# Kernel tuning notes

Hardware: AMD Instinct MI355X
Metric: run time of the kernel (lower is better)

Reference implementation:

```python
import jax, jax.numpy as jnp
import numpy as np

B, T, N, D = 4, 128, 512, 32
CHEB_K, EMB, HEADS, TA_LAYERS, GCN_NUM, TCN_BLOCKS, KSIZE = 3, 10, 2, 2, 3, 3, 3


def setup_inputs() -> dict:
    key = jax.random.key(0)
    ks = jax.random.split(key, 12)
    x = jax.random.normal(ks[0], (B, T, N, D), jnp.float32)
    init_state = jnp.zeros((1, B, N, D), jnp.float32)  # unused by forward, kept for signature fidelity
    node_embeddings = jax.random.normal(ks[1], (N, EMB), jnp.float32)
    a = jax.random.uniform(ks[2], (N, N), jnp.float32)
    a = 0.5 * (a + a.T)
    adj = a / jnp.sum(a, axis=1, keepdims=True)  # row-normalized dense adjacency
    s = 0.05
    gcn_w = jax.random.normal(ks[3], (GCN_NUM, EMB, CHEB_K, D, D), jnp.float32) * s
    gcn_b = jax.random.normal(ks[4], (GCN_NUM, EMB, D), jnp.float32) * s
    tcn_w1 = jax.random.normal(ks[5], (TCN_BLOCKS, D, D, KSIZE), jnp.float32) * s
    tcn_b1 = jnp.zeros((TCN_BLOCKS, D), jnp.float32)
    tcn_w2 = jax.random.normal(ks[6], (TCN_BLOCKS, D, D, KSIZE), jnp.float32) * s
    tcn_b2 = jnp.zeros((TCN_BLOCKS, D), jnp.float32)
    ta_wq = jax.random.normal(ks[7], (TA_LAYERS, D, D), jnp.float32) * s
    ta_wk = jax.random.normal(ks[8], (TA_LAYERS, D, D), jnp.float32) * s
    ta_wv = jax.random.normal(ks[9], (TA_LAYERS, D, D), jnp.float32) * s
    ta_wo = jax.random.normal(ks[10], (TA_LAYERS, D, D), jnp.float32) * s
    ta_g = jnp.ones((TA_LAYERS, D), jnp.float32)
    ta_b = jnp.zeros((TA_LAYERS, D), jnp.float32)
    return dict(x=x, init_state=init_state, node_embeddings=node_embeddings, adj=adj,
                gcn_w=gcn_w, gcn_b=gcn_b, tcn_w1=tcn_w1, tcn_b1=tcn_b1, tcn_w2=tcn_w2,
                tcn_b2=tcn_b2, ta_wq=ta_wq, ta_wk=ta_wk, ta_wv=ta_wv, ta_wo=ta_wo,
                ta_g=ta_g, ta_b=ta_b)


def _cheb_supports(adj, k):
    I = jnp.eye(adj.shape[0], dtype=adj.dtype)
    s = [I, adj]
    for _ in range(2, k):
        s.append(2.0 * (adj @ s[-1]) - s[-2])
    return jnp.stack(s[:k])  # (k, N, N)


def _emb_gcn(h, supports, E, wp, bp):
    # h: (B,T,N,C); supports: (k,N,N); E: (N,EMB); wp: (EMB,k,C,O); bp: (EMB,O)
    xg = jnp.einsum('knm,btmc->btknc', supports, h)
    W = jnp.einsum('ne,ekco->nkco', E, wp)       # per-node Chebyshev weights
    bias = E @ bp                                 # (N,O)
    return jnp.einsum('btknc,nkco->btno', xg, W) + bias


def _causal_conv(y, w, b, dil):
    # y: (BN, C, T); w: (O, C, K)
    pad = (w.shape[-1] - 1) * dil
    out = jax.lax.conv_general_dilated(y, w, (1,), [(pad, 0)], rhs_dilation=(dil,),
                                       dimension_numbers=('NCH', 'OIH', 'NCH'))
    return out + b[None, :, None]


def _temporal_block(y, w1, b1, w2, b2, dil):
    o = jax.nn.relu(_causal_conv(y, w1, b1, dil))
    o = jax.nn.relu(_causal_conv(o, w2, b2, dil))
    return jax.nn.relu(o + y)  # residual (in_ch == out_ch)


def _layernorm(h, g, b):
    mu = jnp.mean(h, -1, keepdims=True)
    var = jnp.var(h, -1, keepdims=True)
    return (h - mu) * jax.lax.rsqrt(var + 1e-5) * g + b


def _attn_layer(h, wq, wk, wv, wo, g, b):
    # h: (BN, T, D) temporal self-attention
    bn, t, d = h.shape
    dh = d // HEADS
    scale = 1.0 / float(np.sqrt(dh))
    q = (h @ wq).reshape(bn, t, HEADS, dh)
    k = (h @ wk).reshape(bn, t, HEADS, dh)
    v = (h @ wv).reshape(bn, t, HEADS, dh)
    a = jax.nn.softmax(jnp.einsum('bqhd,bkhd->bhqk', q, k) * scale, axis=-1)
    o = jnp.einsum('bhqk,bkhd->bqhd', a, v).reshape(bn, t, d) @ wo
    return _layernorm(h + o, g, b)


def reference(x, init_state, node_embeddings, adj, gcn_w, gcn_b, tcn_w1, tcn_b1,
              tcn_w2, tcn_b2, ta_wq, ta_wk, ta_wv, ta_wo, ta_g, ta_b):
    supports = _cheb_supports(adj, CHEB_K)
    h = x
    for i in range(GCN_NUM):  # 3 stacked EmbGCN layers, vectorized over time
        h = _emb_gcn(h, supports, node_embeddings, gcn_w[i], gcn_b[i])
    b, t, n, d = h.shape
    y = jnp.transpose(h, (0, 2, 3, 1)).reshape(b * n, d, t)  # (BN, D, T)
    for i in range(TCN_BLOCKS):  # dilations 1,2,4
        y = _temporal_block(y, tcn_w1[i], tcn_b1[i], tcn_w2[i], tcn_b2[i], 2 ** i)
    h2 = jnp.transpose(y.reshape(b, n, d, t), (0, 1, 3, 2)).reshape(b * n, t, d)
    for i in range(TA_LAYERS):
        h2 = _attn_layer(h2, ta_wq[i], ta_wk[i], ta_wv[i], ta_wo[i], ta_g[i], ta_b[i])
    return jnp.transpose(h2.reshape(b, n, t, d), (0, 2, 1, 3))  # (B,T,N,D)
```

## Files before the change

kernel.cpp:

```cpp
#include <hip/hip_runtime.h>
#include <hip/hip_bf16.h>


typedef __attribute__((ext_vector_type(8))) short short8;
typedef __attribute__((ext_vector_type(4))) short short4v;
typedef __attribute__((ext_vector_type(4))) float float4v;

#define MFMA32(a, b, c) __builtin_amdgcn_mfma_f32_16x16x32_bf16((a), (b), (c), 0, 0, 0)
#if defined(__has_builtin)
#if __has_builtin(__builtin_amdgcn_mfma_f32_16x16x16_bf16)
#define MFMA16A(a, b, c) __builtin_amdgcn_mfma_f32_16x16x16_bf16((a), (b), (c), 0, 0, 0)
#endif
#endif
#ifndef MFMA16A
#define MFMA16A(a, b, c) __builtin_amdgcn_mfma_f32_16x16x16bf16_1k((a), (b), (c), 0, 0, 0)
#endif

#if defined(__has_builtin)
#if __has_builtin(__builtin_amdgcn_exp2f)
#define EXP2F(x) __builtin_amdgcn_exp2f(x)
#endif
#endif
#ifndef EXP2F
#define EXP2F(x) exp2f(x)
#endif

typedef const __attribute__((address_space(1))) unsigned int* gas_ptr;
typedef __attribute__((address_space(3))) unsigned int* las_ptr;
__device__ __forceinline__ void glds16(const void* g, void* l) {
  __builtin_amdgcn_global_load_lds((gas_ptr)g, (las_ptr)l, 16, 0, 0);
}

__device__ __forceinline__ unsigned short f2b(float f) {
  unsigned int x = __float_as_uint(f);
  unsigned int r = (x + 0x7fffu + ((x >> 16) & 1u)) >> 16;
  return (unsigned short)r;
}
__device__ __forceinline__ float b2f(unsigned short u) {
  return __uint_as_float(((unsigned int)u) << 16);
}
__device__ __forceinline__ unsigned int f2b2(float lo, float hi) {
  union { __hip_bfloat162 h; unsigned int u; } cv;
  cv.h = __float22bfloat162_rn(make_float2(lo, hi));
  return cv.u;
}
__device__ __forceinline__ ushort4 f2b4(float a, float b, float c, float d) {
  union { unsigned int u[2]; ushort4 s; } cv;
  cv.u[0] = f2b2(a, b);
  cv.u[1] = f2b2(c, d);
  return cv.s;
}

__global__ void __launch_bounds__(256) prep_supports(
    const float* __restrict__ adj, unsigned short* __restrict__ Sb) {
  __shared__ float arow[512];
  int n = blockIdx.x, tid = threadIdx.x;
  for (int m = tid; m < 512; m += 256) {
    float v = adj[n * 512 + m];
    arow[m] = v;
    Sb[n * 512 + m] = f2b(v);
  }
  __syncthreads();
  for (int m = tid; m < 512; m += 256) {
    float acc = 0.f;
    for (int p = 0; p < 512; ++p) acc += arow[p] * adj[p * 512 + m];
    Sb[(512 + n) * 512 + m] = f2b(2.f * acc - (m == n ? 1.f : 0.f));
  }
}

__global__ void __launch_bounds__(256) prep_w_kernel(
    const float* __restrict__ emb, const float* __restrict__ gw,
    const float* __restrict__ gb,
    unsigned short* __restrict__ W8, float* __restrict__ biasn) {
  int bid = blockIdx.x;
  int i = bid >> 9, n = bid & 511, tid = threadIdx.x;
  float ev[10];
#pragma unroll
  for (int e = 0; e < 10; ++e) ev[e] = emb[n * 10 + e];
  for (int idx = tid; idx < 3072; idx += 256) {
    int s = idx >> 10, c = (idx >> 5) & 31, o = idx & 31;
    float acc = 0.f;
#pragma unroll
    for (int e = 0; e < 10; ++e) acc += ev[e] * gw[(i * 10 + e) * 3072 + idx];
    W8[((i * 512 + n) * 3 + s) * 1024 + (c >> 3) * 256 + o * 8 + (c & 7)] =
        f2b(acc);
  }
  if (tid < 32) {
    float acc = 0.f;
#pragma unroll
    for (int e = 0; e < 10; ++e) acc += ev[e] * gb[(i * 10 + e) * 32 + tid];
    biasn[(i * 512 + n) * 32 + tid] = acc;
  }
}

__global__ void __launch_bounds__(256) prep_tw(
    const float* __restrict__ w1g, const float* __restrict__ w2g,
    unsigned short* __restrict__ Wt) {
  int bid = blockIdx.x;
  int blk = bid >> 1, conv = bid & 1;
  const float* w = (conv ? w2g : w1g) + blk * 3072;
  for (int idx = threadIdx.x; idx < 3072; idx += 256) {
    int kk = idx >> 10, rem = idx & 1023;
    int o = rem >> 5, c = rem & 31;
    Wt[bid * 3072 + idx] = f2b(w[o * 96 + c * 3 + kk]);
  }
}

__global__ void __launch_bounds__(256) prep_attn_w(
    const float* __restrict__ wqg, const float* __restrict__ wkg,
    const float* __restrict__ wvg, const float* __restrict__ wog,
    unsigned short* __restrict__ Wf) {
  int idx = blockIdx.x * 256 + threadIdx.x;
  if (idx >= 8192) return;
  int L = idx >> 12;
  int mat = (idx >> 10) & 3;
  int nt = (idx >> 9) & 1;
  int lane = (idx >> 3) & 63;
  int j = idx & 7;
  int quad = lane >> 4, l15 = lane & 15;
  const float* base =
      (mat == 0 ? wqg : mat == 1 ? wkg : mat == 2 ? wvg : wog) + L * 1024;
  float v = base[(quad * 8 + j) * 32 + nt * 16 + l15];
  if (mat == 0) v *= 0.36067376022224085f;
  Wf[idx] = f2b(v);
}

__global__ void __launch_bounds__(256) conv_x(
    const float* __restrict__ x, unsigned short* __restrict__ H8,
    unsigned short* __restrict__ Hrm) {
  int bid = blockIdx.x;
  int nblk = bid >> 3, part = bid & 7;
  int tid = threadIdx.x;
  for (int qq = tid; qq < 2048; qq += 256) {
    int q = part * 2048 + qq;
    int bt = q >> 5, c = q & 31;
    const float* xb = x + bt * 16384 + nblk * 256 + c;
    float f[8];
#pragma unroll
    for (int s = 0; s < 8; ++s) f[s] = xb[s * 32];
    union { unsigned int u[4]; uint4 v; } pk;
    pk.u[0] = f2b2(f[0], f[1]);
    pk.u[1] = f2b2(f[2], f[3]);
    pk.u[2] = f2b2(f[4], f[5]);
    pk.u[3] = f2b2(f[6], f[7]);
    *(uint4*)&H8[nblk * 131072 + q * 8] = pk.v;
  }
  for (int qq = tid; qq < 2048; qq += 256) {
    int q = part * 2048 + qq;
    int s = q >> 11, e0 = (q & 2047) * 8;
    int bt = e0 >> 5, c0 = e0 & 31;
    const float* xb = x + bt * 16384 + (nblk * 8 + s) * 32 + c0;
    float4 v0 = *(const float4*)&xb[0];
    float4 v1 = *(const float4*)&xb[4];
    union { unsigned int u[4]; uint4 v; } pk;
    pk.u[0] = f2b2(v0.x, v0.y);
    pk.u[1] = f2b2(v0.z, v0.w);
    pk.u[2] = f2b2(v1.x, v1.y);
    pk.u[3] = f2b2(v1.z, v1.w);
    *(uint4*)&Hrm[(nblk * 8 + s) * 16384 + e0] = pk.v;
  }
}

__global__ void __launch_bounds__(256) gcn_phaseA(
    const unsigned short* __restrict__ Sb,
    const unsigned short* __restrict__ H8,
    unsigned short* __restrict__ G) {
  __shared__ unsigned short As[2][128 * 32];
  __shared__ unsigned short Bs[2][4096];
  int bid0 = blockIdx.x;
  int nb = (bid0 & 7) * 128 + (bid0 >> 3);
  int mt = nb & 7, jt = nb >> 3;
  int m0 = mt * 128, j0 = jt * 128;
  int tid = threadIdx.x;
  int wave = tid >> 6, lane = tid & 63;
  int wm = wave >> 1, wj = wave & 1;
  int l15 = lane & 15, quad = lane >> 4;
  float4v acc[4][4];
#pragma unroll
  for (int a = 0; a < 4; ++a)
#pragma unroll
    for (int b = 0; b < 4; ++b) acc[a][b] = (float4v)0.f;
#pragma unroll
  for (int p = 0; p < 2; ++p) {
    int q = tid + p * 256;
    int m = q >> 2;
    int c8 = (q & 3) ^ ((q >> 3) & 3);
    glds16(&Sb[(m0 + m) * 512 + c8 * 8], &As[0][q * 8]);
  }
  {
    const unsigned short* hb = H8 + j0 * 8;
#pragma unroll
    for (int p = 0; p < 2; ++p) {
      int q = tid + p * 256;
      glds16(&hb[(q >> 7) * 131072 + (q & 127) * 8], &Bs[0][q * 8]);
    }
  }
  __syncthreads();
#pragma unroll 2
  for (int it = 0; it < 16; ++it) {
    int cur = it & 1;
    if (it < 15) {
      int ncn = (it + 1) * 32;
#pragma unroll
      for (int p = 0; p < 2; ++p) {
        int q = tid + p * 256;
        int m = q >> 2;
        int c8 = (q & 3) ^ ((q >> 3) & 3);
        glds16(&Sb[(m0 + m) * 512 + ncn + c8 * 8], &As[cur ^ 1][q * 8]);
      }
      const unsigned short* hb = H8 + (ncn >> 3) * 131072 + j0 * 8;
#pragma unroll
      for (int p = 0; p < 2; ++p) {
        int q = tid + p * 256;
        glds16(&hb[(q >> 7) * 131072 + (q & 127) * 8], &Bs[cur ^ 1][q * 8]);
      }
    }
    short8 af[4], bfr[4];
#pragma unroll
    for (int mi = 0; mi < 4; ++mi) {
      int row = wm * 64 + mi * 16 + l15;
      int c8 = quad ^ ((row >> 1) & 3);
      af[mi] = *(const short8*)&As[cur][row * 32 + c8 * 8];
    }
#pragma unroll
    for (int ji = 0; ji < 4; ++ji)
      bfr[ji] =
          *(const short8*)&Bs[cur][quad * 1024 + (wj * 64 + ji * 16 + l15) * 8];
#pragma unroll
    for (int mi = 0; mi < 4; ++mi)
#pragma unroll
      for (int ji = 0; ji < 4; ++ji)
        acc[mi][ji] = MFMA32(af[mi], bfr[ji], acc[mi][ji]);
    __syncthreads();
  }
#pragma unroll
  for (int mi = 0; mi < 4; ++mi)
#pragma unroll
    for (int ji = 0; ji < 4; ++ji) {
      int j = j0 + wj * 64 + ji * 16 + l15;
#pragma unroll
      for (int r = 0; r < 4; ++r) {
        int m = m0 + wm * 64 + mi * 16 + quad * 4 + r;
        G[m * 16384 + j] = f2b(acc[mi][ji][r]);
      }
    }
}

__global__ void __launch_bounds__(256) gcn_phaseB(
    const unsigned short* __restrict__ Hrm, const unsigned short* __restrict__ G,
    const unsigned short* __restrict__ W8, const float* __restrict__ biasn,
    unsigned short* __restrict__ H8out, unsigned short* __restrict__ Hrmout,
    unsigned short* __restrict__ tcnout) {
  int bid = blockIdx.x;
  int n = bid >> 1, bh = bid & 1;
  int tid = threadIdx.x;
  int lane = tid & 63, wave = tid >> 6, l15 = lane & 15, quad = lane >> 4;
  short8 wb[3][2];
#pragma unroll
  for (int s = 0; s < 3; ++s)
#pragma unroll
    for (int nt = 0; nt < 2; ++nt)
      wb[s][nt] = *(const short8*)&W8[(n * 3 + s) * 1024 + quad * 256 +
                                      (nt * 16 + l15) * 8];
  float b0 = biasn[n * 32 + l15], b1 = biasn[n * 32 + 16 + l15];
  int n8base = (n >> 3) * 131072 + (n & 7);
#pragma unroll
  for (int mi = 0; mi < 4; ++mi) {
    int bt0 = bh * 256 + wave * 64 + mi * 16;
    int btl = bt0 + l15;
    short8 a0 = *(const short8*)&Hrm[n * 16384 + btl * 32 + quad * 8];
    short8 a1 = *(const short8*)&G[n * 16384 + btl * 32 + quad * 8];
    short8 a2 = *(const short8*)&G[(512 + n) * 16384 + btl * 32 + quad * 8];
    float4v acc0 = MFMA32(a0, wb[0][0], (float4v)0.f);
    acc0 = MFMA32(a1, wb[1][0], acc0);
    acc0 = MFMA32(a2, wb[2][0], acc0);
    float4v acc1 = MFMA32(a0, wb[0][1], (float4v)0.f);
    acc1 = MFMA32(a1, wb[1][1], acc1);
    acc1 = MFMA32(a2, wb[2][1], acc1);
#pragma unroll
    for (int r = 0; r < 4; ++r) {
      int bt = bt0 + quad * 4 + r;
      unsigned short v0 = f2b(acc0[r] + b0);
      unsigned short v1 = f2b(acc1[r] + b1);
      if (tcnout) {
        int bb = bt >> 7, t = bt & 127;
        int o0 = l15, o1 = 16 + l15;
        tcnout[n * 16384 + bb * 4096 + (o0 >> 3) * 1024 + t * 8 + (o0 & 7)] = v0;
        tcnout[n * 16384 + bb * 4096 + (o1 >> 3) * 1024 + t * 8 + (o1 & 7)] = v1;
      } else {
        H8out[n8base + (bt * 32 + l15) * 8] = v0;
        H8out[n8base + (bt * 32 + 16 + l15) * 8] = v1;
        Hrmout[n * 16384 + bt * 32 + l15] = v0;
        Hrmout[n * 16384 + bt * 32 + 16 + l15] = v1;
      }
    }
  }
}

__global__ void __launch_bounds__(256) tcn_kernel(
    const unsigned short* __restrict__ Yin, unsigned short* __restrict__ yout,
    const unsigned short* __restrict__ Wt,
    const float* __restrict__ b1g, const float* __restrict__ b2g) {
  __shared__ unsigned short Y8[4][4352];
  __shared__ unsigned short O8[4][4352];
  int tid = threadIdx.x, wave = tid >> 6, lane = tid & 63;
  int l15 = lane & 15, quad = lane >> 4;
  int n = blockIdx.x, b = wave;
  unsigned short* y8 = &Y8[wave][0];
  unsigned short* o8 = &O8[wave][0];
  {
    int cg = lane >> 4, t = (lane >> 1) & 7, half = lane & 1;
    ushort4 z = {0, 0, 0, 0};
    *(ushort4*)&y8[(cg * 136 + t) * 8 + half * 4] = z;
    *(ushort4*)&o8[(cg * 136 + t) * 8 + half * 4] = z;
  }
  const unsigned short* src = Yin + n * 16384 + b * 4096;
#pragma unroll
  for (int p = 0; p < 8; ++p) {
    int e = p * 64 + lane;
    int cg = e >> 7, t = e & 127;
    *(uint4*)&y8[(cg * 136 + t + 8) * 8] = *(const uint4*)&src[e * 8];
  }
  for (int blk = 0; blk < 3; ++blk) {
    int dil = 1 << blk;
    for (int conv = 0; conv < 2; ++conv) {
      const unsigned short* wbase = Wt + ((blk * 2 + conv) * 3) * 1024;
      short8 af[2][3];
#pragma unroll
      for (int mt = 0; mt < 2; ++mt)
#pragma unroll
        for (int kk = 0; kk < 3; ++kk)
          af[mt][kk] = *(const short8*)&wbase[kk * 1024 +
                                              (mt * 16 + l15) * 32 + quad * 8];
      const float* bias = (conv ? b2g : b1g) + blk * 32;
      float4 bs0 = *(const float4*)&bias[quad * 4];
      float4 bs1 = *(const float4*)&bias[16 + quad * 4];
      float bb0[4] = {bs0.x, bs0.y, bs0.z, bs0.w};
      float bb1[4] = {bs1.x, bs1.y, bs1.z, bs1.w};
      const unsigned short* rbuf = conv ? o8 : y8;
#pragma unroll 2
      for (int nt = 0; nt < 8; ++nt) {
        float4v acc0 = (float4v)0.f, acc1 = (float4v)0.f;
#pragma unroll
        for (int kk = 0; kk < 3; ++kk) {
          int tb = nt * 16 + l15 + 8 - (2 - kk) * dil;
          short8 bf = *(const short8*)&rbuf[(quad * 136 + tb) * 8];
          acc0 = MFMA32(af[0][kk], bf, acc0);
          acc1 = MFMA32(af[1][kk], bf, acc1);
        }
        int t8 = nt * 16 + l15 + 8;
        int og0 = (quad >> 1), ci0 = (quad & 1) * 4;
        if (conv == 0) {
          ushort4 w0 = f2b4(fmaxf(acc0[0] + bb0[0], 0.f),
                            fmaxf(acc0[1] + bb0[1], 0.f),
                            fmaxf(acc0[2] + bb0[2], 0.f),
                            fmaxf(acc0[3] + bb0[3], 0.f));
          ushort4 w1 = f2b4(fmaxf(acc1[0] + bb1[0], 0.f),
                            fmaxf(acc1[1] + bb1[1], 0.f),
                            fmaxf(acc1[2] + bb1[2], 0.f),
                            fmaxf(acc1[3] + bb1[3], 0.f));
          *(ushort4*)&o8[((og0)*136 + t8) * 8 + ci0] = w0;
          *(ushort4*)&o8[((2 + og0) * 136 + t8) * 8 + ci0] = w1;
        } else {
          ushort4 y0 = *(const ushort4*)&y8[((og0)*136 + t8) * 8 + ci0];
          ushort4 y1 = *(const ushort4*)&y8[((2 + og0) * 136 + t8) * 8 + ci0];
          ushort4 w0 = f2b4(
              fmaxf(fmaxf(acc0[0] + bb0[0], 0.f) + b2f(y0.x), 0.f),
              fmaxf(fmaxf(acc0[1] + bb0[1], 0.f) + b2f(y0.y), 0.f),
              fmaxf(fmaxf(acc0[2] + bb0[2], 0.f) + b2f(y0.z), 0.f),
              fmaxf(fmaxf(acc0[3] + bb0[3], 0.f) + b2f(y0.w), 0.f));
          ushort4 w1 = f2b4(
              fmaxf(fmaxf(acc1[0] + bb1[0], 0.f) + b2f(y1.x), 0.f),
              fmaxf(fmaxf(acc1[1] + bb1[1], 0.f) + b2f(y1.y), 0.f),
              fmaxf(fmaxf(acc1[2] + bb1[2], 0.f) + b2f(y1.z), 0.f),
              fmaxf(fmaxf(acc1[3] + bb1[3], 0.f) + b2f(y1.w), 0.f));
          *(ushort4*)&y8[((og0)*136 + t8) * 8 + ci0] = w0;
          *(ushort4*)&y8[((2 + og0) * 136 + t8) * 8 + ci0] = w1;
        }
      }
    }
  }
  unsigned short* dst = yout + n * 16384 + b * 4096;
#pragma unroll
  for (int p = 0; p < 8; ++p) {
    int e = p * 64 + lane;
    int og = e >> 7, t = e & 127;
    *(uint4*)&dst[t * 32 + og * 8] = *(const uint4*)&y8[(og * 136 + t + 8) * 8];
  }
}

__global__ void __launch_bounds__(256) attn_kernel(
    const unsigned short* __restrict__ yin,
    float* __restrict__ outp,
    const unsigned short* __restrict__ Wf,
    const float* __restrict__ gg, const float* __restrict__ bgb) {
  __shared__ unsigned short hfrag[4096];
  __shared__ unsigned short KbOb[5120];
  __shared__ unsigned short QT[32 * 136];
  __shared__ unsigned short VT[32 * 136];
  int bn = blockIdx.x, tid = threadIdx.x;
  int b = bn >> 9, n = bn & 511;
  int lane = tid & 63, wave = tid >> 6;
  int l15 = lane & 15, quad = lane >> 4;
  int mt0 = wave * 2;

  const unsigned short* src = yin + n * 16384 + b * 4096;
  for (int q = tid; q < 512; q += 256) {
    int t = ((q >> 6) << 4) | (q & 15);
    int cb = (q >> 4) & 3;
    glds16(&src[(t * 4 + cb) * 8], &hfrag[q * 8]);
  }

  for (int L = 0; L < 2; ++L) {
    short8 wf[4][2];
#pragma unroll
    for (int mat = 0; mat < 4; ++mat)
#pragma unroll
      for (int nt = 0; nt < 2; ++nt)
        wf[mat][nt] =
            *(const short8*)&Wf[(((L * 4 + mat) * 2 + nt) * 64 + lane) * 8];
    __syncthreads();
#pragma unroll
    for (int mm = 0; mm < 2; ++mm) {
      int mtq = mt0 + mm;
      short8 af = *(const short8*)&hfrag[(mtq * 4 + quad) * 128 + l15 * 8];
      int tbase = mtq * 16 + quad * 4;
#pragma unroll
      for (int nt = 0; nt < 2; ++nt) {
        float4v qa = MFMA32(af, wf[0][nt], (float4v)0.f);
        float4v ka = MFMA32(af, wf[1][nt], (float4v)0.f);
        float4v va = MFMA32(af, wf[2][nt], (float4v)0.f);
        int d = nt * 16 + l15;
#pragma unroll
        for (int r = 0; r < 4; ++r) KbOb[(tbase + r) * 36 + d] = f2b(ka[r]);
        *(ushort4*)&QT[d * 136 + tbase] = f2b4(qa[0], qa[1], qa[2], qa[3]);
        *(ushort4*)&VT[d * 136 + tbase] = f2b4(va[0], va[1], va[2], va[3]);
      }
    }
    __syncthreads();
    float4v oaccT[2][2];
#pragma unroll
    for (int mm = 0; mm < 2; ++mm)
#pragma unroll
      for (int hh = 0; hh < 2; ++hh) oaccT[mm][hh] = (float4v)0.f;
    for (int hh = 0; hh < 2; ++hh) {
#pragma unroll
      for (int mm = 0; mm < 2; ++mm) {
        int mtq = mt0 + mm;
        short4v qb;
#pragma unroll
        for (int jj = 0; jj < 4; ++jj)
          qb[jj] = (short)QT[(hh * 16 + quad * 4 + jj) * 136 + mtq * 16 + l15];
        float4v sacc[8];
#pragma unroll
        for (int st = 0; st < 8; ++st) {
          short4v ka = *(const short4v*)&KbOb[(st * 16 + l15) * 36 + hh * 16 +
                                              quad * 4];
          sacc[st] = MFMA16A(ka, qb, (float4v)0.f);
        }
        float tmx[8];
#pragma unroll
        for (int st = 0; st < 8; ++st)
          tmx[st] = fmaxf(fmaxf(sacc[st][0], sacc[st][1]),
                          fmaxf(sacc[st][2], sacc[st][3]));
        float mx = fmaxf(fmaxf(fmaxf(tmx[0], tmx[1]), fmaxf(tmx[2], tmx[3])),
                         fmaxf(fmaxf(tmx[4], tmx[5]), fmaxf(tmx[6], tmx[7])));
        mx = fmaxf(mx, __shfl_xor(mx, 16));
        mx = fmaxf(mx, __shfl_xor(mx, 32));
        float ps[8];
#pragma unroll
        for (int st = 0; st < 8; ++st) {
#pragma unroll
          for (int r = 0; r < 4; ++r) sacc[st][r] = EXP2F(sacc[st][r] - mx);
          ps[st] = (sacc[st][0] + sacc[st][1]) + (sacc[st][2] + sacc[st][3]);
        }
        float sum = ((ps[0] + ps[1]) + (ps[2] + ps[3])) +
                    ((ps[4] + ps[5]) + (ps[6] + ps[7]));
        sum += __shfl_xor(sum, 16);
        sum += __shfl_xor(sum, 32);
        float inv = 1.f / sum;
#pragma unroll
        for (int st = 0; st < 8; ++st) {
          union { unsigned int u[2]; short4v s; } pv;
          pv.u[0] = f2b2(sacc[st][0], sacc[st][1]);
          pv.u[1] = f2b2(sacc[st][2], sacc[st][3]);
          short4v va = *(const short4v*)&VT[(hh * 16 + l15) * 136 + st * 16 +
                                            quad * 4];
          oaccT[mm][hh] = MFMA16A(va, pv.s, oaccT[mm][hh]);
        }
#pragma unroll
        for (int r = 0; r < 4; ++r) oaccT[mm][hh][r] *= inv;
      }
    }
    __syncthreads();
#pragma unroll
    for (int mm = 0; mm < 2; ++mm) {
      int mtq = mt0 + mm;
#pragma unroll
      for (int hh = 0; hh < 2; ++hh)
        *(ushort4*)&KbOb[(mtq * 16 + l15) * 40 + hh * 16 + quad * 4] =
            f2b4(oaccT[mm][hh][0], oaccT[mm][hh][1], oaccT[mm][hh][2],
                 oaccT[mm][hh][3]);
    }
    float gam0 = gg[L * 32 + l15], bet0 = bgb[L * 32 + l15];
    float gam1 = gg[L * 32 + 16 + l15], bet1 = bgb[L * 32 + 16 + l15];
#pragma unroll
    for (int mm = 0; mm < 2; ++mm) {
      int mtq = mt0 + mm;
      short8 ofa = *(const short8*)&KbOb[(mtq * 16 + l15) * 40 + quad * 8];
      float4v racc0 = MFMA32(ofa, wf[3][0], (float4v)0.f);
      float4v racc1 = MFMA32(ofa, wf[3][1], (float4v)0.f);
      int hi0 = (mtq * 4 + (l15 >> 3)) * 128 + (l15 & 7);
      int hi1 = (mtq * 4 + 2 + (l15 >> 3)) * 128 + (l15 & 7);
#pragma unroll
      for (int r = 0; r < 4; ++r) {
        int t = mtq * 16 + quad * 4 + r;
        int ro = (quad * 4 + r) * 8;
        float v0 = racc0[r] + b2f(hfrag[hi0 + ro]);
        float v1 = racc1[r] + b2f(hfrag[hi1 + ro]);
        float s = v0 + v1;
        for (int m = 1; m < 16; m <<= 1) s += __shfl_xor(s, m);
        float mu = s * 0.03125f;
        float d0 = v0 - mu, d1 = v1 - mu;
        float q = d0 * d0 + d1 * d1;
        for (int m = 1; m < 16; m <<= 1) q += __shfl_xor(q, m);
        float rs = rsqrtf(q * 0.03125f + 1e-5f);
        float y0 = d0 * rs * gam0 + bet0;
        float y1 = d1 * rs * gam1 + bet1;
        if (L == 0) {
          hfrag[hi0 + ro] = f2b(y0);
          hfrag[hi1 + ro] = f2b(y1);
        } else {
          outp[((b * 128 + t) * 512 + n) * 32 + l15] = y0;
          outp[((b * 128 + t) * 512 + n) * 32 + 16 + l15] = y1;
        }
      }
    }
  }
}

extern "C" void kernel_launch(void* const* d_in, const int* in_sizes, int n_in,
                              void* d_out, int out_size, void* d_ws, size_t ws_size,
                              hipStream_t stream) {
  const float* x    = (const float*)d_in[0];
  const float* emb  = (const float*)d_in[2];
  const float* adj  = (const float*)d_in[3];
  const float* gw   = (const float*)d_in[4];
  const float* gb   = (const float*)d_in[5];
  const float* tw1  = (const float*)d_in[6];
  const float* tb1  = (const float*)d_in[7];
  const float* tw2  = (const float*)d_in[8];
  const float* tb2  = (const float*)d_in[9];
  const float* wq   = (const float*)d_in[10];
  const float* wk   = (const float*)d_in[11];
  const float* wv   = (const float*)d_in[12];
  const float* wo   = (const float*)d_in[13];
  const float* tg   = (const float*)d_in[14];
  const float* tbb  = (const float*)d_in[15];
  float* outp = (float*)d_out;

  char* p = (char*)d_ws;
  unsigned short* Sb  = (unsigned short*)p; p += 1048576;
  unsigned short* W8  = (unsigned short*)p; p += 9437184;
  float* biasn        = (float*)p;          p += 196608;
  unsigned short* G   = (unsigned short*)p; p += 33554432;
  unsigned short* H8a = (unsigned short*)p; p += 16777216;
  unsigned short* H8b = (unsigned short*)p; p += 16777216;
  unsigned short* Hra = (unsigned short*)p; p += 16777216;
  unsigned short* Hrb = (unsigned short*)p; p += 16777216;
  unsigned short* Wt  = (unsigned short*)p; p += 36864;
  unsigned short* Wf  = (unsigned short*)p; p += 16384;

  prep_supports<<<dim3(512), dim3(256), 0, stream>>>(adj, Sb);
  prep_w_kernel<<<dim3(1536), dim3(256), 0, stream>>>(emb, gw, gb, W8, biasn);
  prep_tw<<<dim3(6), dim3(256), 0, stream>>>(tw1, tw2, Wt);
  prep_attn_w<<<dim3(32), dim3(256), 0, stream>>>(wq, wk, wv, wo, Wf);
  conv_x<<<dim3(512), dim3(256), 0, stream>>>(x, H8a, Hra);

  gcn_phaseA<<<dim3(1024), dim3(256), 0, stream>>>(Sb, H8a, G);
  gcn_phaseB<<<dim3(1024), dim3(256), 0, stream>>>(
      Hra, G, W8, biasn, H8b, Hrb, (unsigned short*)nullptr);
  gcn_phaseA<<<dim3(1024), dim3(256), 0, stream>>>(Sb, H8b, G);
  gcn_phaseB<<<dim3(1024), dim3(256), 0, stream>>>(
      Hrb, G, W8 + 1572864, biasn + 16384, H8a, Hra, (unsigned short*)nullptr);
  gcn_phaseA<<<dim3(1024), dim3(256), 0, stream>>>(Sb, H8a, G);
  gcn_phaseB<<<dim3(1024), dim3(256), 0, stream>>>(
      Hra, G, W8 + 3145728, biasn + 32768, (unsigned short*)nullptr,
      (unsigned short*)nullptr, H8b);

  tcn_kernel<<<dim3(512), dim3(256), 0, stream>>>(H8b, H8a, Wt, tb1, tb2);
  attn_kernel<<<dim3(2048), dim3(256), 0, stream>>>(H8a, outp, Wf, tg, tbb);
}
```

Baseline: 415.5 us.

## Merge prep kernels into one launch and compute adj squared with MFMA

Folds the five preprocessing kernels (supports, GCN weights, TCN weights, attention weights, input conversion) into a single kernel that dispatches on block index ranges, cutting four launches. The adj@adj product for the second Chebyshev support moves from a scalar fp32 loop to a tiled bf16 MFMA GEMM over 16 blocks. f2b now uses the hardware bf16 conversion path. The squared support is computed from bf16-rounded inputs, so it is less precise, and only 16 blocks do the GEMM, which may leave it on the critical path.

```diff
diff --git a/kernel.cpp b/kernel.cpp
--- a/kernel.cpp
+++ b/kernel.cpp
@@ -31,18 +31,16 @@
   __builtin_amdgcn_global_load_lds((gas_ptr)g, (las_ptr)l, 16, 0, 0);
 }
 
-__device__ __forceinline__ unsigned short f2b(float f) {
-  unsigned int x = __float_as_uint(f);
-  unsigned int r = (x + 0x7fffu + ((x >> 16) & 1u)) >> 16;
-  return (unsigned short)r;
-}
-__device__ __forceinline__ float b2f(unsigned short u) {
-  return __uint_as_float(((unsigned int)u) << 16);
-}
 __device__ __forceinline__ unsigned int f2b2(float lo, float hi) {
   union { __hip_bfloat162 h; unsigned int u; } cv;
   cv.h = __float22bfloat162_rn(make_float2(lo, hi));
   return cv.u;
+}
+__device__ __forceinline__ unsigned short f2b(float f) {
+  return (unsigned short)f2b2(f, f);
+}
+__device__ __forceinline__ float b2f(unsigned short u) {
+  return __uint_as_float(((unsigned int)u) << 16);
 }
 __device__ __forceinline__ ushort4 f2b4(float a, float b, float c, float d) {
   union { unsigned int u[2]; ushort4 s; } cv;
@@ -51,113 +49,168 @@
   return cv.s;
 }
 
-__global__ void __launch_bounds__(256) prep_supports(
-    const float* __restrict__ adj, unsigned short* __restrict__ Sb) {
-  __shared__ float arow[512];
-  int n = blockIdx.x, tid = threadIdx.x;
-  for (int m = tid; m < 512; m += 256) {
-    float v = adj[n * 512 + m];
-    arow[m] = v;
-    Sb[n * 512 + m] = f2b(v);
-  }
-  __syncthreads();
-  for (int m = tid; m < 512; m += 256) {
-    float acc = 0.f;
-    for (int p = 0; p < 512; ++p) acc += arow[p] * adj[p * 512 + m];
-    Sb[(512 + n) * 512 + m] = f2b(2.f * acc - (m == n ? 1.f : 0.f));
-  }
-}
-
-__global__ void __launch_bounds__(256) prep_w_kernel(
+__global__ void __launch_bounds__(256) prep_all(
+    const float* __restrict__ adj, unsigned short* __restrict__ Sb,
     const float* __restrict__ emb, const float* __restrict__ gw,
-    const float* __restrict__ gb,
-    unsigned short* __restrict__ W8, float* __restrict__ biasn) {
-  int bid = blockIdx.x;
-  int i = bid >> 9, n = bid & 511, tid = threadIdx.x;
-  float ev[10];
-#pragma unroll
-  for (int e = 0; e < 10; ++e) ev[e] = emb[n * 10 + e];
-  for (int idx = tid; idx < 3072; idx += 256) {
-    int s = idx >> 10, c = (idx >> 5) & 31, o = idx & 31;
-    float acc = 0.f;
-#pragma unroll
-    for (int e = 0; e < 10; ++e) acc += ev[e] * gw[(i * 10 + e) * 3072 + idx];
-    W8[((i * 512 + n) * 3 + s) * 1024 + (c >> 3) * 256 + o * 8 + (c & 7)] =
-        f2b(acc);
-  }
-  if (tid < 32) {
-    float acc = 0.f;
-#pragma unroll
-    for (int e = 0; e < 10; ++e) acc += ev[e] * gb[(i * 10 + e) * 32 + tid];
-    biasn[(i * 512 + n) * 32 + tid] = acc;
-  }
-}
-
-__global__ void __launch_bounds__(256) prep_tw(
+    const float* __restrict__ gb, unsigned short* __restrict__ W8,
+    float* __restrict__ biasn,
     const float* __restrict__ w1g, const float* __restrict__ w2g,
-    unsigned short* __restrict__ Wt) {
-  int bid = blockIdx.x;
-  int blk = bid >> 1, conv = bid & 1;
-  const float* w = (conv ? w2g : w1g) + blk * 3072;
-  for (int idx = threadIdx.x; idx < 3072; idx += 256) {
-    int kk = idx >> 10, rem = idx & 1023;
-    int o = rem >> 5, c = rem & 31;
-    Wt[bid * 3072 + idx] = f2b(w[o * 96 + c * 3 + kk]);
-  }
-}
-
-__global__ void __launch_bounds__(256) prep_attn_w(
+    unsigned short* __restrict__ Wt,
     const float* __restrict__ wqg, const float* __restrict__ wkg,
     const float* __restrict__ wvg, const float* __restrict__ wog,
-    unsigned short* __restrict__ Wf) {
-  int idx = blockIdx.x * 256 + threadIdx.x;
-  if (idx >= 8192) return;
-  int L = idx >> 12;
-  int mat = (idx >> 10) & 3;
-  int nt = (idx >> 9) & 1;
-  int lane = (idx >> 3) & 63;
-  int j = idx & 7;
-  int quad = lane >> 4, l15 = lane & 15;
-  const float* base =
-      (mat == 0 ? wqg : mat == 1 ? wkg : mat == 2 ? wvg : wog) + L * 1024;
-  float v = base[(quad * 8 + j) * 32 + nt * 16 + l15];
-  if (mat == 0) v *= 0.36067376022224085f;
-  Wf[idx] = f2b(v);
-}
-
-__global__ void __launch_bounds__(256) conv_x(
+    unsigned short* __restrict__ Wf,
     const float* __restrict__ x, unsigned short* __restrict__ H8,
     unsigned short* __restrict__ Hrm) {
-  int bid = blockIdx.x;
-  int nblk = bid >> 3, part = bid & 7;
-  int tid = threadIdx.x;
-  for (int qq = tid; qq < 2048; qq += 256) {
-    int q = part * 2048 + qq;
-    int bt = q >> 5, c = q & 31;
-    const float* xb = x + bt * 16384 + nblk * 256 + c;
-    float f[8];
-#pragma unroll
-    for (int s = 0; s < 8; ++s) f[s] = xb[s * 32];
-    union { unsigned int u[4]; uint4 v; } pk;
-    pk.u[0] = f2b2(f[0], f[1]);
-    pk.u[1] = f2b2(f[2], f[3]);
-    pk.u[2] = f2b2(f[4], f[5]);
-    pk.u[3] = f2b2(f[6], f[7]);
-    *(uint4*)&H8[nblk * 131072 + q * 8] = pk.v;
-  }
-  for (int qq = tid; qq < 2048; qq += 256) {
-    int q = part * 2048 + qq;
-    int s = q >> 11, e0 = (q & 2047) * 8;
-    int bt = e0 >> 5, c0 = e0 & 31;
-    const float* xb = x + bt * 16384 + (nblk * 8 + s) * 32 + c0;
-    float4 v0 = *(const float4*)&xb[0];
-    float4 v1 = *(const float4*)&xb[4];
-    union { unsigned int u[4]; uint4 v; } pk;
-    pk.u[0] = f2b2(v0.x, v0.y);
-    pk.u[1] = f2b2(v0.z, v0.w);
-    pk.u[2] = f2b2(v1.x, v1.y);
-    pk.u[3] = f2b2(v1.z, v1.w);
-    *(uint4*)&Hrm[(nblk * 8 + s) * 16384 + e0] = pk.v;
+  __shared__ unsigned short Asq[128 * 40];
+  __shared__ unsigned short Bsq[128 * 40];
+  int bid = blockIdx.x, tid = threadIdx.x;
+
+  if (bid < 64) {
+    int base = bid * 4096;
+#pragma unroll
+    for (int it = 0; it < 4; ++it) {
+      int e = base + it * 1024 + tid * 4;
+      float4 v = *(const float4*)&adj[e];
+      union { unsigned int u[2]; ushort4 s; } pk;
+      pk.u[0] = f2b2(v.x, v.y);
+      pk.u[1] = f2b2(v.z, v.w);
+      *(ushort4*)&Sb[e] = pk.s;
+    }
+    return;
+  }
+  if (bid < 80) {
+    int tb = bid - 64;
+    int mt = tb >> 2, jt = tb & 3;
+    int m0 = mt * 128, j0 = jt * 128;
+    int wave = tid >> 6, lane = tid & 63;
+    int wm = wave >> 1, wj = wave & 1;
+    int l15 = lane & 15, quad = lane >> 4;
+    float4v acc[4][4];
+#pragma unroll
+    for (int a = 0; a < 4; ++a)
+#pragma unroll
+      for (int b = 0; b < 4; ++b) acc[a][b] = (float4v)0.f;
+    for (int kt = 0; kt < 512; kt += 32) {
+#pragma unroll
+      for (int p = 0; p < 16; ++p) {
+        int idx = p * 256 + tid;
+        int m = idx >> 5, k = idx & 31;
+        Asq[m * 40 + k] = f2b(adj[(m0 + m) * 512 + kt + k]);
+      }
+#pragma unroll
+      for (int p = 0; p < 16; ++p) {
+        int idx = p * 256 + tid;
+        int k = idx >> 7, j = idx & 127;
+        Bsq[j * 40 + k] = f2b(adj[(kt + k) * 512 + j0 + j]);
+      }
+      __syncthreads();
+      short8 af[4], bfr[4];
+#pragma unroll
+      for (int mi = 0; mi < 4; ++mi)
+        af[mi] = *(const short8*)&Asq[(wm * 64 + mi * 16 + l15) * 40 + quad * 8];
+#pragma unroll
+      for (int ji = 0; ji < 4; ++ji)
+        bfr[ji] = *(const short8*)&Bsq[(wj * 64 + ji * 16 + l15) * 40 + quad * 8];
+#pragma unroll
+      for (int mi = 0; mi < 4; ++mi)
+#pragma unroll
+        for (int ji = 0; ji < 4; ++ji)
+          acc[mi][ji] = MFMA32(af[mi], bfr[ji], acc[mi][ji]);
+      __syncthreads();
+    }
+#pragma unroll
+    for (int mi = 0; mi < 4; ++mi)
+#pragma unroll
+      for (int ji = 0; ji < 4; ++ji) {
+        int j = j0 + wj * 64 + ji * 16 + l15;
+#pragma unroll
+        for (int r = 0; r < 4; ++r) {
+          int m = m0 + wm * 64 + mi * 16 + quad * 4 + r;
+          Sb[(512 + m) * 512 + j] =
+              f2b(2.f * acc[mi][ji][r] - (m == j ? 1.f : 0.f));
+        }
+      }
+    return;
+  }
+  if (bid < 1616) {
+    int b2 = bid - 80;
+    int i = b2 >> 9, n = b2 & 511;
+    float ev[10];
+#pragma unroll
+    for (int e = 0; e < 10; ++e) ev[e] = emb[n * 10 + e];
+    for (int idx = tid; idx < 3072; idx += 256) {
+      int s = idx >> 10, c = (idx >> 5) & 31, o = idx & 31;
+      float acc = 0.f;
+#pragma unroll
+      for (int e = 0; e < 10; ++e) acc += ev[e] * gw[(i * 10 + e) * 3072 + idx];
+      W8[((i * 512 + n) * 3 + s) * 1024 + (c >> 3) * 256 + o * 8 + (c & 7)] =
+          f2b(acc);
+    }
+    if (tid < 32) {
+      float acc = 0.f;
+#pragma unroll
+      for (int e = 0; e < 10; ++e) acc += ev[e] * gb[(i * 10 + e) * 32 + tid];
+      biasn[(i * 512 + n) * 32 + tid] = acc;
+    }
+    return;
+  }
+  if (bid < 1622) {
+    int b2 = bid - 1616;
+    int blk = b2 >> 1, conv = b2 & 1;
+    const float* w = (conv ? w2g : w1g) + blk * 3072;
+    for (int idx = tid; idx < 3072; idx += 256) {
+      int kk = idx >> 10, rem = idx & 1023;
+      int o = rem >> 5, c = rem & 31;
+      Wt[b2 * 3072 + idx] = f2b(w[o * 96 + c * 3 + kk]);
+    }
+    return;
+  }
+  if (bid < 1654) {
+    int idx = (bid - 1622) * 256 + tid;
+    int L = idx >> 12;
+    int mat = (idx >> 10) & 3;
+    int nt = (idx >> 9) & 1;
+    int lane = (idx >> 3) & 63;
+    int j = idx & 7;
+    int quad = lane >> 4, l15 = lane & 15;
+    const float* base =
+        (mat == 0 ? wqg : mat == 1 ? wkg : mat == 2 ? wvg : wog) + L * 1024;
+    float v = base[(quad * 8 + j) * 32 + nt * 16 + l15];
+    if (mat == 0) v *= 0.36067376022224085f;
+    Wf[idx] = f2b(v);
+    return;
+  }
+  {
+    int b2 = bid - 1654;
+    int nblk = b2 >> 3, part = b2 & 7;
+    for (int qq = tid; qq < 2048; qq += 256) {
+      int q = part * 2048 + qq;
+      int bt = q >> 5, c = q & 31;
+      const float* xb = x + bt * 16384 + nblk * 256 + c;
+      float f[8];
+#pragma unroll
+      for (int s = 0; s < 8; ++s) f[s] = xb[s * 32];
+      union { unsigned int u[4]; uint4 v; } pk;
+      pk.u[0] = f2b2(f[0], f[1]);
+      pk.u[1] = f2b2(f[2], f[3]);
+      pk.u[2] = f2b2(f[4], f[5]);
+      pk.u[3] = f2b2(f[6], f[7]);
+      *(uint4*)&H8[nblk * 131072 + q * 8] = pk.v;
+    }
+    for (int qq = tid; qq < 2048; qq += 256) {
+      int q = part * 2048 + qq;
+      int s = q >> 11, e0 = (q & 2047) * 8;
+      int bt = e0 >> 5, c0 = e0 & 31;
+      const float* xb = x + bt * 16384 + (nblk * 8 + s) * 32 + c0;
+      float4 v0 = *(const float4*)&xb[0];
+      float4 v1 = *(const float4*)&xb[4];
+      union { unsigned int u[4]; uint4 v; } pk;
+      pk.u[0] = f2b2(v0.x, v0.y);
+      pk.u[1] = f2b2(v0.z, v0.w);
+      pk.u[2] = f2b2(v1.x, v1.y);
+      pk.u[3] = f2b2(v1.z, v1.w);
+      *(uint4*)&Hrm[(nblk * 8 + s) * 16384 + e0] = pk.v;
+    }
   }
 }
 
@@ -571,11 +624,9 @@
   unsigned short* Wt  = (unsigned short*)p; p += 36864;
   unsigned short* Wf  = (unsigned short*)p; p += 16384;
 
-  prep_supports<<<dim3(512), dim3(256), 0, stream>>>(adj, Sb);
-  prep_w_kernel<<<dim3(1536), dim3(256), 0, stream>>>(emb, gw, gb, W8, biasn);
-  prep_tw<<<dim3(6), dim3(256), 0, stream>>>(tw1, tw2, Wt);
-  prep_attn_w<<<dim3(32), dim3(256), 0, stream>>>(wq, wk, wv, wo, Wf);
-  conv_x<<<dim3(512), dim3(256), 0, stream>>>(x, H8a, Hra);
+  prep_all<<<dim3(2166), dim3(256), 0, stream>>>(
+      adj, Sb, emb, gw, gb, W8, biasn, tw1, tw2, Wt, wq, wk, wv, wo, Wf,
+      x, H8a, Hra);
 
   gcn_phaseA<<<dim3(1024), dim3(256), 0, stream>>>(Sb, H8a, G);
   gcn_phaseB<<<dim3(1024), dim3(256), 0, stream>>>(
```

After: 384.9 us. 1.08x faster.
